# Kernel optimization log

Hardware: AMD Instinct MI355X
Metric: run time of the kernel (lower is better)

Reference implementation:

```python
import jax, jax.numpy as jnp
import numpy as np

N_NODES = 50000
N_EDGES = 800000
N_FEAT = 128
HIDDEN = 64
N_LAYERS = 3
N_GRAPHS = 512
N_CLASSES = 10
BN_EPS = 1e-5


def setup_inputs() -> dict:
    key = jax.random.key(0)
    ks = jax.random.split(key, 16)
    s = 1.0 / np.sqrt(HIDDEN)
    inp = {
        "x": jax.random.normal(ks[0], (N_NODES, N_FEAT), dtype=jnp.float32),
        "edge_index": jax.random.randint(ks[1], (2, N_EDGES), 0, N_NODES, dtype=jnp.int32),
        "batch": jnp.sort(jax.random.randint(ks[2], (N_NODES,), 0, N_GRAPHS, dtype=jnp.int32)),
        "enc_w": jax.random.normal(ks[3], (N_FEAT, HIDDEN), dtype=jnp.float32) / np.sqrt(N_FEAT),
        "enc_b": jnp.zeros((HIDDEN,), dtype=jnp.float32),
        "eps": jnp.zeros((N_LAYERS,), dtype=jnp.float32),
        "conv_w1": jax.random.normal(ks[4], (N_LAYERS, HIDDEN, HIDDEN), dtype=jnp.float32) * s,
        "conv_b1": jnp.zeros((N_LAYERS, HIDDEN), dtype=jnp.float32),
        "conv_w2": jax.random.normal(ks[5], (N_LAYERS, HIDDEN, HIDDEN), dtype=jnp.float32) * s,
        "conv_b2": jnp.zeros((N_LAYERS, HIDDEN), dtype=jnp.float32),
        "bn_gamma": jnp.ones((N_LAYERS, HIDDEN), dtype=jnp.float32),
        "bn_beta": jnp.zeros((N_LAYERS, HIDDEN), dtype=jnp.float32),
        "lin_w": jax.random.normal(ks[6], (HIDDEN, N_CLASSES), dtype=jnp.float32) * s,
        "lin_b": jnp.zeros((N_CLASSES,), dtype=jnp.float32),
    }
    return inp


def reference(x, edge_index, batch, enc_w, enc_b, eps, conv_w1, conv_b1,
              conv_w2, conv_b2, bn_gamma, bn_beta, lin_w, lin_b):
    n = x.shape[0]
    src, dst = edge_index[0], edge_index[1]
    h = x @ enc_w + enc_b  # [N, H] encoder
    for l in range(N_LAYERS):
        # GINConv: sum-aggregate neighbor features, add (1+eps)*self, 2-layer MLP
        agg = jax.ops.segment_sum(h[src], dst, num_segments=n)
        z = (1.0 + eps[l]) * h + agg
        z = jnp.maximum(z @ conv_w1[l] + conv_b1[l], 0.0) @ conv_w2[l] + conv_b2[l]
        # BatchNorm1d (batch statistics) + ReLU; dropout omitted (eval mode)
        mean = jnp.mean(z, axis=0)
        var = jnp.mean(jnp.square(z - mean), axis=0)
        z = (z - mean) * jax.lax.rsqrt(var + BN_EPS) * bn_gamma[l] + bn_beta[l]
        h = jnp.maximum(z, 0.0)
    # global mean pool over graphs
    pooled = jax.ops.segment_sum(h, batch, num_segments=N_GRAPHS)
    counts = jax.ops.segment_sum(jnp.ones((n,), dtype=h.dtype), batch, num_segments=N_GRAPHS)
    pooled = pooled / jnp.maximum(counts, 1.0)[:, None]
    return pooled @ lin_w + lin_b  # [N_GRAPHS, N_CLASSES]
```

## Files before the change

### kernel.cpp

```cpp
#include <hip/hip_runtime.h>

#define N_NODES   50000
#define N_EDGES   800000
#define N_FEAT    128
#define HIDDEN    64
#define N_LAYERS  3
#define N_GRAPHS  512
#define N_CLASSES 10
#define BN_EPS    1e-5f
#define SCAN_BLK  196
#define PITCH     68
#define EPITCH    132
#define LWAVES    8

__global__ __launch_bounds__(512, 6) void enc_kernel(
    const float* __restrict__ x, const float* __restrict__ w,
    const float* __restrict__ b, float* __restrict__ h)
{
    __shared__ __align__(16) float wT[HIDDEN * EPITCH];
    __shared__ __align__(16) float xb[LWAVES][4][N_FEAT];
    for (int i = threadIdx.x; i < N_FEAT * HIDDEN; i += 512) {
        int k = i >> 6, c = i & 63;
        wT[c * EPITCH + k] = w[i];
    }
    const int col = threadIdx.x & 63;
    const int wv  = threadIdx.x >> 6;
    const float bias = b[col];
    __syncthreads();
    const int nwaves = gridDim.x * LWAVES;
    for (int grp = blockIdx.x * LWAVES + wv; grp < N_NODES / 4; grp += nwaves) {
        const int nbase = grp * 4;
        #pragma unroll
        for (int n = 0; n < 4; ++n) {
            xb[wv][n][col]      = x[(size_t)(nbase + n) * N_FEAT + col];
            xb[wv][n][64 + col] = x[(size_t)(nbase + n) * N_FEAT + 64 + col];
        }
        float o0 = bias, o1 = bias, o2 = bias, o3 = bias;
        #pragma unroll 4
        for (int kc = 0; kc < N_FEAT / 4; ++kc) {
            float4 w4 = *(const float4*)&wT[col * EPITCH + 4 * kc];
            float4 z0 = *(const float4*)&xb[wv][0][4 * kc];
            float4 z1 = *(const float4*)&xb[wv][1][4 * kc];
            float4 z2 = *(const float4*)&xb[wv][2][4 * kc];
            float4 z3 = *(const float4*)&xb[wv][3][4 * kc];
            o0 = fmaf(w4.x, z0.x, fmaf(w4.y, z0.y, fmaf(w4.z, z0.z, fmaf(w4.w, z0.w, o0))));
            o1 = fmaf(w4.x, z1.x, fmaf(w4.y, z1.y, fmaf(w4.z, z1.z, fmaf(w4.w, z1.w, o1))));
            o2 = fmaf(w4.x, z2.x, fmaf(w4.y, z2.y, fmaf(w4.z, z2.z, fmaf(w4.w, z2.w, o2))));
            o3 = fmaf(w4.x, z3.x, fmaf(w4.y, z3.y, fmaf(w4.z, z3.z, fmaf(w4.w, z3.w, o3))));
        }
        h[(size_t)(nbase + 0) * HIDDEN + col] = o0;
        h[(size_t)(nbase + 1) * HIDDEN + col] = o1;
        h[(size_t)(nbase + 2) * HIDDEN + col] = o2;
        h[(size_t)(nbase + 3) * HIDDEN + col] = o3;
    }
}

__global__ __launch_bounds__(256) void hist_kernel(const int* __restrict__ ei,
                                                   int* __restrict__ deg)
{
    int e = blockIdx.x * 256 + threadIdx.x;
    if (e < N_EDGES) atomicAdd(&deg[ei[N_EDGES + e]], 1);
}

__global__ __launch_bounds__(256) void scan1_kernel(const int* __restrict__ deg,
                                                    int* __restrict__ row_start,
                                                    int* __restrict__ bsum)
{
    __shared__ int s[256];
    const int tid = threadIdx.x;
    const int gid = blockIdx.x * 256 + tid;
    int v = (gid < N_NODES) ? deg[gid] : 0;
    s[tid] = v;
    __syncthreads();
    for (int off = 1; off < 256; off <<= 1) {
        int t = (tid >= off) ? s[tid - off] : 0;
        __syncthreads();
        if (tid >= off) s[tid] += t;
        __syncthreads();
    }
    if (gid < N_NODES) row_start[gid] = s[tid] - v;
    if (tid == 255) bsum[blockIdx.x] = s[255];
}

__global__ __launch_bounds__(256) void scan2_kernel(int* __restrict__ bsum,
                                                    int* __restrict__ row_start)
{
    __shared__ int s[256];
    const int tid = threadIdx.x;
    int v = (tid < SCAN_BLK) ? bsum[tid] : 0;
    s[tid] = v;
    __syncthreads();
    for (int off = 1; off < 256; off <<= 1) {
        int t = (tid >= off) ? s[tid - off] : 0;
        __syncthreads();
        if (tid >= off) s[tid] += t;
        __syncthreads();
    }
    if (tid < SCAN_BLK) bsum[tid] = s[tid] - v;
    if (tid == 255) row_start[N_NODES] = s[255];
}

__global__ __launch_bounds__(256) void scan3_kernel(int* __restrict__ row_start,
                                                    const int* __restrict__ bsum,
                                                    int* __restrict__ cursor)
{
    int gid = blockIdx.x * 256 + threadIdx.x;
    if (gid < N_NODES) {
        int v = row_start[gid] + bsum[blockIdx.x];
        row_start[gid] = v;
        cursor[gid] = v;
    }
}

__global__ __launch_bounds__(256) void fill_kernel(const int* __restrict__ ei,
                                                   int* __restrict__ cursor,
                                                   int* __restrict__ csr_src)
{
    int e = blockIdx.x * 256 + threadIdx.x;
    if (e >= N_EDGES) return;
    int d = ei[N_EDGES + e];
    int pos = atomicAdd(&cursor[d], 1);
    csr_src[pos] = ei[e];
}

template<bool HASBN>
__global__ __launch_bounds__(512, 6) void layer_kernel(
    const float* __restrict__ hin, const int* __restrict__ csr_src,
    const int* __restrict__ row_start,
    const float* __restrict__ stats_prev, const float* __restrict__ gamma,
    const float* __restrict__ beta,
    const float* __restrict__ eps, int layer,
    const float* __restrict__ w1, const float* __restrict__ b1,
    const float* __restrict__ w2, const float* __restrict__ b2,
    float* __restrict__ hout, float* __restrict__ stats_cur)
{
    __shared__ __align__(16) float wT1[HIDDEN * PITCH];
    __shared__ __align__(16) float wT2[HIDDEN * PITCH];
    __shared__ __align__(16) float zb[LWAVES][4][HIDDEN];
    for (int i = threadIdx.x; i < HIDDEN * HIDDEN; i += 512) {
        int k = i >> 6, c = i & 63;
        wT1[c * PITCH + k] = w1[i];
        wT2[c * PITCH + k] = w2[i];
    }
    const int col = threadIdx.x & 63;
    const int wv  = threadIdx.x >> 6;
    float A = 1.0f, Bc = 0.0f;
    if (HASBN) {
        const float invN = 1.0f / (float)N_NODES;
        float mean = stats_prev[col] * invN;
        float var  = stats_prev[HIDDEN + col] * invN - mean * mean;
        float inv  = rsqrtf(fmaxf(var, 0.f) + BN_EPS);
        A = inv * gamma[col];
        Bc = beta[col] - mean * A;
    }
    const float sf  = 1.0f + eps[layer];
    const float b1c = b1[col], b2c = b2[col];
    __syncthreads();

    float s = 0.f, s2 = 0.f;
    const int nwaves = gridDim.x * LWAVES;
    for (int grp = blockIdx.x * LWAVES + wv; grp < N_NODES / 4; grp += nwaves) {
        const int nbase = grp * 4;
        for (int n = 0; n < 4; ++n) {
            const int node = nbase + n;
            const int s0 = row_start[node];
            const int s1 = row_start[node + 1];
            float v = hin[(size_t)node * HIDDEN + col];
            if (HASBN) v = fmaxf(fmaf(v, A, Bc), 0.f);
            float a0 = sf * v, a1 = 0.f, a2 = 0.f, a3 = 0.f;
            for (int jb = s0; jb < s1; jb += 64) {
                int m = s1 - jb; if (m > 64) m = 64;
                int idx = csr_src[jb + (col < m ? col : m - 1)];
                int j = 0;
                for (; j + 4 <= m; j += 4) {
                    int i0 = __shfl(idx, j + 0), i1 = __shfl(idx, j + 1);
                    int i2 = __shfl(idx, j + 2), i3 = __shfl(idx, j + 3);
                    float u0 = hin[(size_t)i0 * HIDDEN + col];
                    float u1 = hin[(size_t)i1 * HIDDEN + col];
                    float u2 = hin[(size_t)i2 * HIDDEN + col];
                    float u3 = hin[(size_t)i3 * HIDDEN + col];
                    if (HASBN) {
                        u0 = fmaxf(fmaf(u0, A, Bc), 0.f);
                        u1 = fmaxf(fmaf(u1, A, Bc), 0.f);
                        u2 = fmaxf(fmaf(u2, A, Bc), 0.f);
                        u3 = fmaxf(fmaf(u3, A, Bc), 0.f);
                    }
                    a0 += u0; a1 += u1; a2 += u2; a3 += u3;
                }
                for (; j < m; ++j) {
                    int i0 = __shfl(idx, j);
                    float u = hin[(size_t)i0 * HIDDEN + col];
                    if (HASBN) u = fmaxf(fmaf(u, A, Bc), 0.f);
                    a0 += u;
                }
            }
            zb[wv][n][col] = (a0 + a1) + (a2 + a3);
        }
        float o0 = b1c, o1 = b1c, o2 = b1c, o3 = b1c;
        #pragma unroll 4
        for (int kc = 0; kc < HIDDEN / 4; ++kc) {
            float4 w4 = *(const float4*)&wT1[col * PITCH + 4 * kc];
            float4 z0 = *(const float4*)&zb[wv][0][4 * kc];
            float4 z1 = *(const float4*)&zb[wv][1][4 * kc];
            float4 z2 = *(const float4*)&zb[wv][2][4 * kc];
            float4 z3 = *(const float4*)&zb[wv][3][4 * kc];
            o0 = fmaf(w4.x, z0.x, fmaf(w4.y, z0.y, fmaf(w4.z, z0.z, fmaf(w4.w, z0.w, o0))));
            o1 = fmaf(w4.x, z1.x, fmaf(w4.y, z1.y, fmaf(w4.z, z1.z, fmaf(w4.w, z1.w, o1))));
            o2 = fmaf(w4.x, z2.x, fmaf(w4.y, z2.y, fmaf(w4.z, z2.z, fmaf(w4.w, z2.w, o2))));
            o3 = fmaf(w4.x, z3.x, fmaf(w4.y, z3.y, fmaf(w4.z, z3.z, fmaf(w4.w, z3.w, o3))));
        }
        zb[wv][0][col] = fmaxf(o0, 0.f);
        zb[wv][1][col] = fmaxf(o1, 0.f);
        zb[wv][2][col] = fmaxf(o2, 0.f);
        zb[wv][3][col] = fmaxf(o3, 0.f);
        float p0 = b2c, p1 = b2c, p2 = b2c, p3 = b2c;
        #pragma unroll 4
        for (int kc = 0; kc < HIDDEN / 4; ++kc) {
            float4 w4 = *(const float4*)&wT2[col * PITCH + 4 * kc];
            float4 z0 = *(const float4*)&zb[wv][0][4 * kc];
            float4 z1 = *(const float4*)&zb[wv][1][4 * kc];
            float4 z2 = *(const float4*)&zb[wv][2][4 * kc];
            float4 z3 = *(const float4*)&zb[wv][3][4 * kc];
            p0 = fmaf(w4.x, z0.x, fmaf(w4.y, z0.y, fmaf(w4.z, z0.z, fmaf(w4.w, z0.w, p0))));
            p1 = fmaf(w4.x, z1.x, fmaf(w4.y, z1.y, fmaf(w4.z, z1.z, fmaf(w4.w, z1.w, p1))));
            p2 = fmaf(w4.x, z2.x, fmaf(w4.y, z2.y, fmaf(w4.z, z2.z, fmaf(w4.w, z2.w, p2))));
            p3 = fmaf(w4.x, z3.x, fmaf(w4.y, z3.y, fmaf(w4.z, z3.z, fmaf(w4.w, z3.w, p3))));
        }
        hout[(size_t)(nbase + 0) * HIDDEN + col] = p0;
        hout[(size_t)(nbase + 1) * HIDDEN + col] = p1;
        hout[(size_t)(nbase + 2) * HIDDEN + col] = p2;
        hout[(size_t)(nbase + 3) * HIDDEN + col] = p3;
        s  += ((p0 + p1) + (p2 + p3));
        s2 += ((p0 * p0 + p1 * p1) + (p2 * p2 + p3 * p3));
    }
    __syncthreads();
    float* red = &zb[0][0][0];
    red[threadIdx.x] = s;
    red[512 + threadIdx.x] = s2;
    __syncthreads();
    if (wv == 0) {
        float ts = 0.f, ts2 = 0.f;
        #pragma unroll
        for (int wq = 0; wq < LWAVES; ++wq) {
            ts  += red[wq * 64 + col];
            ts2 += red[512 + wq * 64 + col];
        }
        atomicAdd(&stats_cur[col], ts);
        atomicAdd(&stats_cur[HIDDEN + col], ts2);
    }
}

__device__ __forceinline__ int lbound(const int* __restrict__ a, int n, int v)
{
    int lo = 0, hi = n;
    while (lo < hi) { int m = (lo + hi) >> 1; if (a[m] < v) lo = m + 1; else hi = m; }
    return lo;
}

__global__ __launch_bounds__(256) void pool_kernel(
    const float* __restrict__ hpre, const int* __restrict__ batch,
    const float* __restrict__ stats, const float* __restrict__ gamma,
    const float* __restrict__ beta, float* __restrict__ pooled)
{
    __shared__ int bounds[2];
    __shared__ float red[256];
    const int g = blockIdx.x;
    if (threadIdx.x < 2)
        bounds[threadIdx.x] = lbound(batch, N_NODES, g + threadIdx.x);
    __syncthreads();
    const int start = bounds[0], end = bounds[1];
    const int col = threadIdx.x & 63;
    const int row = threadIdx.x >> 6;
    const float invN = 1.0f / (float)N_NODES;
    float mean = stats[col] * invN;
    float var  = stats[HIDDEN + col] * invN - mean * mean;
    float inv  = rsqrtf(fmaxf(var, 0.f) + BN_EPS);
    float A = inv * gamma[col];
    float B = beta[col] - mean * A;
    float s = 0.f;
    for (int r = start + row; r < end; r += 4)
        s += fmaxf(fmaf(hpre[(size_t)r * HIDDEN + col], A, B), 0.f);
    red[threadIdx.x] = s;
    __syncthreads();
    if (row == 0) {
        float t = red[col] + red[64 + col] + red[128 + col] + red[192 + col];
        pooled[(size_t)g * HIDDEN + col] = t / fmaxf((float)(end - start), 1.0f);
    }
}

__global__ void out_kernel(const float* __restrict__ pooled,
                           const float* __restrict__ w, const float* __restrict__ b,
                           float* __restrict__ out)
{
    int gid = blockIdx.x * blockDim.x + threadIdx.x;
    if (gid >= N_GRAPHS * N_CLASSES) return;
    int g = gid / N_CLASSES;
    int c = gid - g * N_CLASSES;
    float acc = b[c];
    for (int j = 0; j < HIDDEN; ++j)
        acc = fmaf(pooled[(size_t)g * HIDDEN + j], w[j * N_CLASSES + c], acc);
    out[gid] = acc;
}

extern "C" void kernel_launch(void* const* d_in, const int* in_sizes, int n_in,
                              void* d_out, int out_size, void* d_ws, size_t ws_size,
                              hipStream_t stream)
{
    const float* x       = (const float*)d_in[0];
    const int*   ei      = (const int*)d_in[1];
    const int*   batch   = (const int*)d_in[2];
    const float* enc_w   = (const float*)d_in[3];
    const float* enc_b   = (const float*)d_in[4];
    const float* eps     = (const float*)d_in[5];
    const float* conv_w1 = (const float*)d_in[6];
    const float* conv_b1 = (const float*)d_in[7];
    const float* conv_w2 = (const float*)d_in[8];
    const float* conv_b2 = (const float*)d_in[9];
    const float* bn_g    = (const float*)d_in[10];
    const float* bn_b    = (const float*)d_in[11];
    const float* lin_w   = (const float*)d_in[12];
    const float* lin_b   = (const float*)d_in[13];
    float* out = (float*)d_out;

    char* ws = (char*)d_ws;
    const size_t HB = (size_t)N_NODES * HIDDEN * sizeof(float);
    size_t off = 0;
    float* P      = (float*)(ws + off); off += HB;
    float* Q      = (float*)(ws + off); off += HB;
    float* stats  = (float*)(ws + off); off += N_LAYERS * 2 * HIDDEN * sizeof(float);
    float* pooled = (float*)(ws + off); off += (size_t)N_GRAPHS * HIDDEN * sizeof(float);
    int* deg       = (int*)(ws + off); off += 50176 * sizeof(int);
    int* row_start = (int*)(ws + off); off += 50176 * sizeof(int);
    int* cursor    = (int*)(ws + off); off += 50176 * sizeof(int);
    int* bsum      = (int*)(ws + off); off += 256 * sizeof(int);
    int* csr_src   = (int*)(ws + off); off += (size_t)N_EDGES * sizeof(int);

    hipMemsetAsync(deg, 0, N_NODES * sizeof(int), stream);
    hipMemsetAsync(stats, 0, N_LAYERS * 2 * HIDDEN * sizeof(float), stream);

    enc_kernel<<<768, 512, 0, stream>>>(x, enc_w, enc_b, P);

    hist_kernel<<<(N_EDGES + 255) / 256, 256, 0, stream>>>(ei, deg);
    scan1_kernel<<<SCAN_BLK, 256, 0, stream>>>(deg, row_start, bsum);
    scan2_kernel<<<1, 256, 0, stream>>>(bsum, row_start);
    scan3_kernel<<<SCAN_BLK, 256, 0, stream>>>(row_start, bsum, cursor);
    fill_kernel<<<(N_EDGES + 255) / 256, 256, 0, stream>>>(ei, cursor, csr_src);

    const float* curin = P;
    float* curout = Q;
    for (int l = 0; l < N_LAYERS; ++l) {
        const float* w1 = conv_w1 + (size_t)l * HIDDEN * HIDDEN;
        const float* b1 = conv_b1 + (size_t)l * HIDDEN;
        const float* w2 = conv_w2 + (size_t)l * HIDDEN * HIDDEN;
        const float* b2 = conv_b2 + (size_t)l * HIDDEN;
        if (l == 0)
            layer_kernel<false><<<768, 512, 0, stream>>>(
                curin, csr_src, row_start, nullptr, nullptr, nullptr,
                eps, l, w1, b1, w2, b2, curout, stats);
        else
            layer_kernel<true><<<768, 512, 0, stream>>>(
                curin, csr_src, row_start,
                stats + (size_t)(l - 1) * 2 * HIDDEN,
                bn_g + (size_t)(l - 1) * HIDDEN, bn_b + (size_t)(l - 1) * HIDDEN,
                eps, l, w1, b1, w2, b2, curout, stats + (size_t)l * 2 * HIDDEN);
        const float* t = curout; curout = (float*)curin; curin = t;
    }

    pool_kernel<<<N_GRAPHS, 256, 0, stream>>>(
        Q, batch, stats + (size_t)(N_LAYERS - 1) * 2 * HIDDEN,
        bn_g + (size_t)(N_LAYERS - 1) * HIDDEN, bn_b + (size_t)(N_LAYERS - 1) * HIDDEN,
        pooled);
    out_kernel<<<(N_GRAPHS * N_CLASSES + 255) / 256, 256, 0, stream>>>(pooled, lin_w, lin_b, out);
}
```

Baseline: 338.0 us.

## Vectorize neighbor gather to float4 rows and swizzle weight smem layout

The neighbor aggregation now has each quarter-wave load a full 64-float row as float4 per lane, so four neighbors are fetched per instruction. The partial sums are then reduced across quarters with xor shuffles. Weight tiles in shared memory use an XOR swizzle instead of padded pitches to avoid bank conflicts, and the encoder loads x with float4. Occupancy hints and grid size for the layer kernel are raised to 8 waves per SIMD and 1024 blocks, which may increase register pressure and adds shuffle reduction overhead.

```diff
diff --git a/kernel.cpp b/kernel.cpp
--- a/kernel.cpp
+++ b/kernel.cpp
@@ -9,36 +9,38 @@
 #define N_CLASSES 10
 #define BN_EPS    1e-5f
 #define SCAN_BLK  196
-#define PITCH     68
-#define EPITCH    132
 #define LWAVES    8
+
+__device__ __forceinline__ int swz(int c, int g) { return g ^ (c & 15); }
 
 __global__ __launch_bounds__(512, 6) void enc_kernel(
     const float* __restrict__ x, const float* __restrict__ w,
     const float* __restrict__ b, float* __restrict__ h)
 {
-    __shared__ __align__(16) float wT[HIDDEN * EPITCH];
+    __shared__ __align__(16) float wT[HIDDEN * N_FEAT];
     __shared__ __align__(16) float xb[LWAVES][4][N_FEAT];
     for (int i = threadIdx.x; i < N_FEAT * HIDDEN; i += 512) {
         int k = i >> 6, c = i & 63;
-        wT[c * EPITCH + k] = w[i];
-    }
-    const int col = threadIdx.x & 63;
-    const int wv  = threadIdx.x >> 6;
-    const float bias = b[col];
+        wT[c * 128 + swz(c, k >> 2) * 4 + (k & 3)] = w[i];
+    }
+    const int lane = threadIdx.x & 63;
+    const int wv   = threadIdx.x >> 6;
+    const int sz   = lane & 15;
+    const int r2   = lane >> 5;
+    const int cc   = (lane & 31) * 4;
+    const float bias = b[lane];
     __syncthreads();
     const int nwaves = gridDim.x * LWAVES;
     for (int grp = blockIdx.x * LWAVES + wv; grp < N_NODES / 4; grp += nwaves) {
         const int nbase = grp * 4;
-        #pragma unroll
-        for (int n = 0; n < 4; ++n) {
-            xb[wv][n][col]      = x[(size_t)(nbase + n) * N_FEAT + col];
-            xb[wv][n][64 + col] = x[(size_t)(nbase + n) * N_FEAT + 64 + col];
-        }
+        float4 v0 = *(const float4*)&x[(size_t)(nbase + r2) * N_FEAT + cc];
+        float4 v1 = *(const float4*)&x[(size_t)(nbase + 2 + r2) * N_FEAT + cc];
+        *((float4*)&xb[wv][r2][cc])     = v0;
+        *((float4*)&xb[wv][2 + r2][cc]) = v1;
         float o0 = bias, o1 = bias, o2 = bias, o3 = bias;
-        #pragma unroll 4
+        #pragma unroll 8
         for (int kc = 0; kc < N_FEAT / 4; ++kc) {
-            float4 w4 = *(const float4*)&wT[col * EPITCH + 4 * kc];
+            float4 w4 = *(const float4*)&wT[lane * 128 + ((kc ^ sz) << 2)];
             float4 z0 = *(const float4*)&xb[wv][0][4 * kc];
             float4 z1 = *(const float4*)&xb[wv][1][4 * kc];
             float4 z2 = *(const float4*)&xb[wv][2][4 * kc];
@@ -48,10 +50,10 @@
             o2 = fmaf(w4.x, z2.x, fmaf(w4.y, z2.y, fmaf(w4.z, z2.z, fmaf(w4.w, z2.w, o2))));
             o3 = fmaf(w4.x, z3.x, fmaf(w4.y, z3.y, fmaf(w4.z, z3.z, fmaf(w4.w, z3.w, o3))));
         }
-        h[(size_t)(nbase + 0) * HIDDEN + col] = o0;
-        h[(size_t)(nbase + 1) * HIDDEN + col] = o1;
-        h[(size_t)(nbase + 2) * HIDDEN + col] = o2;
-        h[(size_t)(nbase + 3) * HIDDEN + col] = o3;
+        h[(size_t)(nbase + 0) * HIDDEN + lane] = o0;
+        h[(size_t)(nbase + 1) * HIDDEN + lane] = o1;
+        h[(size_t)(nbase + 2) * HIDDEN + lane] = o2;
+        h[(size_t)(nbase + 3) * HIDDEN + lane] = o3;
     }
 }
 
@@ -124,7 +126,7 @@
 }
 
 template<bool HASBN>
-__global__ __launch_bounds__(512, 6) void layer_kernel(
+__global__ __launch_bounds__(512, 8) void layer_kernel(
     const float* __restrict__ hin, const int* __restrict__ csr_src,
     const int* __restrict__ row_start,
     const float* __restrict__ stats_prev, const float* __restrict__ gamma,
@@ -134,72 +136,101 @@
     const float* __restrict__ w2, const float* __restrict__ b2,
     float* __restrict__ hout, float* __restrict__ stats_cur)
 {
-    __shared__ __align__(16) float wT1[HIDDEN * PITCH];
-    __shared__ __align__(16) float wT2[HIDDEN * PITCH];
+    __shared__ __align__(16) float wT1[HIDDEN * HIDDEN];
+    __shared__ __align__(16) float wT2[HIDDEN * HIDDEN];
     __shared__ __align__(16) float zb[LWAVES][4][HIDDEN];
     for (int i = threadIdx.x; i < HIDDEN * HIDDEN; i += 512) {
         int k = i >> 6, c = i & 63;
-        wT1[c * PITCH + k] = w1[i];
-        wT2[c * PITCH + k] = w2[i];
-    }
-    const int col = threadIdx.x & 63;
-    const int wv  = threadIdx.x >> 6;
-    float A = 1.0f, Bc = 0.0f;
+        int dst = c * 64 + swz(c, k >> 2) * 4 + (k & 3);
+        wT1[dst] = w1[i];
+        wT2[dst] = w2[i];
+    }
+    const int lane = threadIdx.x & 63;
+    const int wv   = threadIdx.x >> 6;
+    const int q    = lane >> 4;
+    const int c4   = (lane & 15) * 4;
+    const int sz   = lane & 15;
+    float Ag[4] = {1.f, 1.f, 1.f, 1.f}, Bg[4] = {0.f, 0.f, 0.f, 0.f};
     if (HASBN) {
         const float invN = 1.0f / (float)N_NODES;
-        float mean = stats_prev[col] * invN;
-        float var  = stats_prev[HIDDEN + col] * invN - mean * mean;
-        float inv  = rsqrtf(fmaxf(var, 0.f) + BN_EPS);
-        A = inv * gamma[col];
-        Bc = beta[col] - mean * A;
+        #pragma unroll
+        for (int t = 0; t < 4; ++t) {
+            float mean = stats_prev[c4 + t] * invN;
+            float var  = stats_prev[HIDDEN + c4 + t] * invN - mean * mean;
+            float inv  = rsqrtf(fmaxf(var, 0.f) + BN_EPS);
+            Ag[t] = inv * gamma[c4 + t];
+            Bg[t] = beta[c4 + t] - mean * Ag[t];
+        }
     }
     const float sf  = 1.0f + eps[layer];
-    const float b1c = b1[col], b2c = b2[col];
+    const float b1c = b1[lane], b2c = b2[lane];
     __syncthreads();
 
     float s = 0.f, s2 = 0.f;
     const int nwaves = gridDim.x * LWAVES;
     for (int grp = blockIdx.x * LWAVES + wv; grp < N_NODES / 4; grp += nwaves) {
         const int nbase = grp * 4;
+        #pragma unroll
         for (int n = 0; n < 4; ++n) {
             const int node = nbase + n;
             const int s0 = row_start[node];
             const int s1 = row_start[node + 1];
-            float v = hin[(size_t)node * HIDDEN + col];
-            if (HASBN) v = fmaxf(fmaf(v, A, Bc), 0.f);
-            float a0 = sf * v, a1 = 0.f, a2 = 0.f, a3 = 0.f;
+            float a0 = 0.f, a1 = 0.f, a2 = 0.f, a3 = 0.f;
             for (int jb = s0; jb < s1; jb += 64) {
                 int m = s1 - jb; if (m > 64) m = 64;
-                int idx = csr_src[jb + (col < m ? col : m - 1)];
-                int j = 0;
-                for (; j + 4 <= m; j += 4) {
-                    int i0 = __shfl(idx, j + 0), i1 = __shfl(idx, j + 1);
-                    int i2 = __shfl(idx, j + 2), i3 = __shfl(idx, j + 3);
-                    float u0 = hin[(size_t)i0 * HIDDEN + col];
-                    float u1 = hin[(size_t)i1 * HIDDEN + col];
-                    float u2 = hin[(size_t)i2 * HIDDEN + col];
-                    float u3 = hin[(size_t)i3 * HIDDEN + col];
+                int idx = csr_src[jb + (lane < m ? lane : m - 1)];
+                int mm = m & ~3;
+                for (int j = 0; j < mm; j += 4) {
+                    int i = __shfl(idx, j + q);
+                    const float* r = &hin[(size_t)i * HIDDEN + c4];
+                    float4 u = *(const float4*)r;
                     if (HASBN) {
-                        u0 = fmaxf(fmaf(u0, A, Bc), 0.f);
-                        u1 = fmaxf(fmaf(u1, A, Bc), 0.f);
-                        u2 = fmaxf(fmaf(u2, A, Bc), 0.f);
-                        u3 = fmaxf(fmaf(u3, A, Bc), 0.f);
+                        u.x = fmaxf(fmaf(u.x, Ag[0], Bg[0]), 0.f);
+                        u.y = fmaxf(fmaf(u.y, Ag[1], Bg[1]), 0.f);
+                        u.z = fmaxf(fmaf(u.z, Ag[2], Bg[2]), 0.f);
+                        u.w = fmaxf(fmaf(u.w, Ag[3], Bg[3]), 0.f);
                     }
-                    a0 += u0; a1 += u1; a2 += u2; a3 += u3;
+                    a0 += u.x; a1 += u.y; a2 += u.z; a3 += u.w;
                 }
-                for (; j < m; ++j) {
-                    int i0 = __shfl(idx, j);
-                    float u = hin[(size_t)i0 * HIDDEN + col];
-                    if (HASBN) u = fmaxf(fmaf(u, A, Bc), 0.f);
-                    a0 += u;
+                int r3 = m & 3;
+                if (r3) {
+                    int sl = mm + q;
+                    int i = __shfl(idx, sl < m ? sl : m - 1);
+                    const float* r = &hin[(size_t)i * HIDDEN + c4];
+                    float4 u = *(const float4*)r;
+                    if (HASBN) {
+                        u.x = fmaxf(fmaf(u.x, Ag[0], Bg[0]), 0.f);
+                        u.y = fmaxf(fmaf(u.y, Ag[1], Bg[1]), 0.f);
+                        u.z = fmaxf(fmaf(u.z, Ag[2], Bg[2]), 0.f);
+                        u.w = fmaxf(fmaf(u.w, Ag[3], Bg[3]), 0.f);
+                    }
+                    if (q < r3) { a0 += u.x; a1 += u.y; a2 += u.z; a3 += u.w; }
                 }
             }
-            zb[wv][n][col] = (a0 + a1) + (a2 + a3);
+            a0 += __shfl_xor(a0, 16); a1 += __shfl_xor(a1, 16);
+            a2 += __shfl_xor(a2, 16); a3 += __shfl_xor(a3, 16);
+            a0 += __shfl_xor(a0, 32); a1 += __shfl_xor(a1, 32);
+            a2 += __shfl_xor(a2, 32); a3 += __shfl_xor(a3, 32);
+            float4 sv = *(const float4*)&hin[(size_t)node * HIDDEN + c4];
+            if (HASBN) {
+                sv.x = fmaxf(fmaf(sv.x, Ag[0], Bg[0]), 0.f);
+                sv.y = fmaxf(fmaf(sv.y, Ag[1], Bg[1]), 0.f);
+                sv.z = fmaxf(fmaf(sv.z, Ag[2], Bg[2]), 0.f);
+                sv.w = fmaxf(fmaf(sv.w, Ag[3], Bg[3]), 0.f);
+            }
+            if (q == 0) {
+                float4 z4;
+                z4.x = fmaf(sf, sv.x, a0);
+                z4.y = fmaf(sf, sv.y, a1);
+                z4.z = fmaf(sf, sv.z, a2);
+                z4.w = fmaf(sf, sv.w, a3);
+                *((float4*)&zb[wv][n][c4]) = z4;
+            }
         }
         float o0 = b1c, o1 = b1c, o2 = b1c, o3 = b1c;
         #pragma unroll 4
         for (int kc = 0; kc < HIDDEN / 4; ++kc) {
-            float4 w4 = *(const float4*)&wT1[col * PITCH + 4 * kc];
+            float4 w4 = *(const float4*)&wT1[lane * 64 + ((kc ^ sz) << 2)];
             float4 z0 = *(const float4*)&zb[wv][0][4 * kc];
             float4 z1 = *(const float4*)&zb[wv][1][4 * kc];
             float4 z2 = *(const float4*)&zb[wv][2][4 * kc];
@@ -209,14 +240,14 @@
             o2 = fmaf(w4.x, z2.x, fmaf(w4.y, z2.y, fmaf(w4.z, z2.z, fmaf(w4.w, z2.w, o2))));
             o3 = fmaf(w4.x, z3.x, fmaf(w4.y, z3.y, fmaf(w4.z, z3.z, fmaf(w4.w, z3.w, o3))));
         }
-        zb[wv][0][col] = fmaxf(o0, 0.f);
-        zb[wv][1][col] = fmaxf(o1, 0.f);
-        zb[wv][2][col] = fmaxf(o2, 0.f);
-        zb[wv][3][col] = fmaxf(o3, 0.f);
+        zb[wv][0][lane] = fmaxf(o0, 0.f);
+        zb[wv][1][lane] = fmaxf(o1, 0.f);
+        zb[wv][2][lane] = fmaxf(o2, 0.f);
+        zb[wv][3][lane] = fmaxf(o3, 0.f);
         float p0 = b2c, p1 = b2c, p2 = b2c, p3 = b2c;
         #pragma unroll 4
         for (int kc = 0; kc < HIDDEN / 4; ++kc) {
-            float4 w4 = *(const float4*)&wT2[col * PITCH + 4 * kc];
+            float4 w4 = *(const float4*)&wT2[lane * 64 + ((kc ^ sz) << 2)];
             float4 z0 = *(const float4*)&zb[wv][0][4 * kc];
             float4 z1 = *(const float4*)&zb[wv][1][4 * kc];
             float4 z2 = *(const float4*)&zb[wv][2][4 * kc];
@@ -226,10 +257,10 @@
             p2 = fmaf(w4.x, z2.x, fmaf(w4.y, z2.y, fmaf(w4.z, z2.z, fmaf(w4.w, z2.w, p2))));
             p3 = fmaf(w4.x, z3.x, fmaf(w4.y, z3.y, fmaf(w4.z, z3.z, fmaf(w4.w, z3.w, p3))));
         }
-        hout[(size_t)(nbase + 0) * HIDDEN + col] = p0;
-        hout[(size_t)(nbase + 1) * HIDDEN + col] = p1;
-        hout[(size_t)(nbase + 2) * HIDDEN + col] = p2;
-        hout[(size_t)(nbase + 3) * HIDDEN + col] = p3;
+        hout[(size_t)(nbase + 0) * HIDDEN + lane] = p0;
+        hout[(size_t)(nbase + 1) * HIDDEN + lane] = p1;
+        hout[(size_t)(nbase + 2) * HIDDEN + lane] = p2;
+        hout[(size_t)(nbase + 3) * HIDDEN + lane] = p3;
         s  += ((p0 + p1) + (p2 + p3));
         s2 += ((p0 * p0 + p1 * p1) + (p2 * p2 + p3 * p3));
     }
@@ -242,11 +273,11 @@
         float ts = 0.f, ts2 = 0.f;
         #pragma unroll
         for (int wq = 0; wq < LWAVES; ++wq) {
-            ts  += red[wq * 64 + col];
-            ts2 += red[512 + wq * 64 + col];
-        }
-        atomicAdd(&stats_cur[col], ts);
-        atomicAdd(&stats_cur[HIDDEN + col], ts2);
+            ts  += red[wq * 64 + lane];
+            ts2 += red[512 + wq * 64 + lane];
+        }
+        atomicAdd(&stats_cur[lane], ts);
+        atomicAdd(&stats_cur[HIDDEN + lane], ts2);
     }
 }
 
@@ -354,11 +385,11 @@
         const float* w2 = conv_w2 + (size_t)l * HIDDEN * HIDDEN;
         const float* b2 = conv_b2 + (size_t)l * HIDDEN;
         if (l == 0)
-            layer_kernel<false><<<768, 512, 0, stream>>>(
+            layer_kernel<false><<<1024, 512, 0, stream>>>(
                 curin, csr_src, row_start, nullptr, nullptr, nullptr,
                 eps, l, w1, b1, w2, b2, curout, stats);
         else
-            layer_kernel<true><<<768, 512, 0, stream>>>(
+            layer_kernel<true><<<1024, 512, 0, stream>>>(
                 curin, csr_src, row_start,
                 stats + (size_t)(l - 1) * 2 * HIDDEN,
                 bn_g + (size_t)(l - 1) * HIDDEN, bn_b + (size_t)(l - 1) * HIDDEN,
```

Measured after the change: 339.1 us. No clear change (+0.3%).
